# Optimization experiments

Hardware: AMD Instinct MI355X
Metric: run time of the kernel (lower is better)

Reference implementation:

```python
import jax, jax.numpy as jnp
import numpy as np

ALPHA = 0.2  # LeakyReLU negative slope
NEG_BIG = -9e15


def setup_inputs() -> dict:
    key = jax.random.key(0)
    k1, k2, k3, k4 = jax.random.split(key, 4)
    bs, N, Fin, Fout = 4, 4096, 256, 256
    inp = jax.random.normal(k1, (bs, N, Fin), dtype=jnp.float32)
    adj = jax.random.randint(k2, (bs, N, N), 0, 2, dtype=jnp.int32)
    W = jax.random.normal(k3, (Fin, Fout), dtype=jnp.float32) * (1.414 / np.sqrt(Fin))
    a = jax.random.normal(k4, (2 * Fout, 1), dtype=jnp.float32) * 0.1
    return {"input": inp, "adj": adj, "W": W, "a": a}


def reference(input, adj, W, a):
    # h: [bs, N, Fout]
    h = jnp.matmul(input, W)
    Fout = W.shape[1]
    a1 = a[:Fout, 0]   # attends to source node i (row of a_input's first half)
    a2 = a[Fout:, 0]   # attends to node j
    # e[b,i,j] = leakyrelu(a1.h_i + a2.h_j); exact decomposition of
    # cat(h_i, h_j) @ a without materializing the [bs, N, N, 2F] tensor.
    f1 = jnp.einsum('bnf,f->bn', h, a1)  # [bs, N]
    f2 = jnp.einsum('bnf,f->bn', h, a2)  # [bs, N]
    e = jax.nn.leaky_relu(f1[:, :, None] + f2[:, None, :], negative_slope=ALPHA)
    logits = jnp.where(adj > 0, e, NEG_BIG)
    # NOTE: original softmaxes over dim=1 (axis of i), faithfully kept.
    attention = jax.nn.softmax(logits, axis=1)
    # dropout p=0.0 (eval mode) -> identity
    h_prime = jnp.matmul(attention, h)  # contract over axis 2
    return jax.nn.elu(h_prime)  # concat=True
```

## Files before the change

kernel.cpp:

```cpp
#include <hip/hip_runtime.h>
#include <cstdint>
#include <cstddef>


#define GAT_ALPHA 0.2f
#define LOG2E 1.4426950408889634f

#if __has_builtin(__builtin_amdgcn_exp2f)
__device__ __forceinline__ float exp2_fast(float x){ return __builtin_amdgcn_exp2f(x); }
#else
__device__ __forceinline__ float exp2_fast(float x){ return exp2f(x); }
#endif

typedef __bf16 bf16x8 __attribute__((ext_vector_type(8)));
typedef __bf16 bf16x4 __attribute__((ext_vector_type(4)));
typedef float  f32x4  __attribute__((ext_vector_type(4)));

__global__ __launch_bounds__(256) void k1_h_gemm(
    const float* __restrict__ inp, const float* __restrict__ W,
    const float* __restrict__ avec, float* __restrict__ h,
    float* __restrict__ f1p, float* __restrict__ f2p)
{
  const int b  = blockIdx.y;
  const int i0 = blockIdx.x * 64;
  const int tid = threadIdx.x;
  const int tr = tid >> 5;
  const int tc = tid & 31;
  __shared__ float Wt[64][256];
  __shared__ float in_t[64][64];
  float acc[8][8];
  #pragma unroll
  for (int r = 0; r < 8; ++r)
    #pragma unroll
    for (int c = 0; c < 8; ++c) acc[r][c] = 0.f;

  const float* inb = inp + (size_t)b * 4096 * 256;
  for (int kt = 0; kt < 4; ++kt) {
    #pragma unroll
    for (int e = 0; e < 16; ++e) {
      int flat4 = e * 256 + tid;
      int kk = flat4 >> 6;
      int ff = (flat4 & 63) * 4;
      *(float4*)&Wt[kk][ff] = *(const float4*)(W + (size_t)(kt*64 + kk) * 256 + ff);
    }
    #pragma unroll
    for (int e = 0; e < 4; ++e) {
      int flat4 = e * 256 + tid;
      int row = flat4 >> 4;
      int col = (flat4 & 15) * 4;
      *(float4*)&in_t[row][col] = *(const float4*)(inb + (size_t)(i0 + row) * 256 + kt*64 + col);
    }
    __syncthreads();
    for (int k = 0; k < 64; ++k) {
      float av[8], bv[8];
      #pragma unroll
      for (int r = 0; r < 8; ++r) av[r] = in_t[tr*8 + r][k];
      float4 b0 = *(float4*)&Wt[k][tc*8];
      float4 b1 = *(float4*)&Wt[k][tc*8 + 4];
      bv[0]=b0.x; bv[1]=b0.y; bv[2]=b0.z; bv[3]=b0.w;
      bv[4]=b1.x; bv[5]=b1.y; bv[6]=b1.z; bv[7]=b1.w;
      #pragma unroll
      for (int r = 0; r < 8; ++r)
        #pragma unroll
        for (int c = 0; c < 8; ++c)
          acc[r][c] = fmaf(av[r], bv[c], acc[r][c]);
    }
    __syncthreads();
  }

  float* hb = h + (size_t)b * 4096 * 256;
  #pragma unroll
  for (int r = 0; r < 8; ++r) {
    int i = i0 + tr*8 + r;
    float4 o0 = make_float4(acc[r][0], acc[r][1], acc[r][2], acc[r][3]);
    float4 o1 = make_float4(acc[r][4], acc[r][5], acc[r][6], acc[r][7]);
    *(float4*)(hb + (size_t)i * 256 + tc*8)     = o0;
    *(float4*)(hb + (size_t)i * 256 + tc*8 + 4) = o1;
  }

  float a1r[8], a2r[8];
  {
    float4 x0 = *(const float4*)(avec + tc*8);
    float4 x1 = *(const float4*)(avec + tc*8 + 4);
    a1r[0]=x0.x; a1r[1]=x0.y; a1r[2]=x0.z; a1r[3]=x0.w;
    a1r[4]=x1.x; a1r[5]=x1.y; a1r[6]=x1.z; a1r[7]=x1.w;
    float4 y0 = *(const float4*)(avec + 256 + tc*8);
    float4 y1 = *(const float4*)(avec + 256 + tc*8 + 4);
    a2r[0]=y0.x; a2r[1]=y0.y; a2r[2]=y0.z; a2r[3]=y0.w;
    a2r[4]=y1.x; a2r[5]=y1.y; a2r[6]=y1.z; a2r[7]=y1.w;
  }
  #pragma unroll
  for (int r = 0; r < 8; ++r) {
    float v1 = 0.f, v2 = 0.f;
    #pragma unroll
    for (int c = 0; c < 8; ++c) { v1 = fmaf(acc[r][c], a1r[c], v1); v2 = fmaf(acc[r][c], a2r[c], v2); }
    #pragma unroll
    for (int off = 16; off >= 1; off >>= 1) {
      v1 += __shfl_xor(v1, off);
      v2 += __shfl_xor(v2, off);
    }
    if (tc == 0) {
      int i = i0 + tr*8 + r;
      f1p[b*4096 + i] = v1 * LOG2E;
      f2p[b*4096 + i] = v2 * LOG2E;
    }
  }
}

__global__ __launch_bounds__(256) void k2_stream(
    const int* __restrict__ adj, const float* __restrict__ f1p, const float* __restrict__ f2p,
    float* __restrict__ Sp, unsigned long long* __restrict__ mask)
{
  const int jt = blockIdx.x, sp = blockIdx.y, b = blockIdx.z;
  const int tid = threadIdx.x;
  const int wv = tid >> 6, lane = tid & 63;
  const int j0 = jt * 1024;
  const int i0 = sp * 64;

  __shared__ float f1s[64];
  if (tid < 64) f1s[tid] = f1p[b*4096 + i0 + tid];
  float f2v[4], s[4];
  #pragma unroll
  for (int g = 0; g < 4; ++g) {
    f2v[g] = f2p[b*4096 + j0 + g*256 + tid];
    s[g] = 0.f;
  }
  __syncthreads();

  const int* adjb = adj + ((size_t)b * 4096 + i0) * 4096 + j0;
  #pragma unroll 4
  for (int ii = 0; ii < 64; ++ii) {
    const float f1v = f1s[ii];
    const int* arow = adjb + (size_t)ii * 4096;
    #pragma unroll
    for (int g = 0; g < 4; ++g) {
      int av = arow[g*256 + tid];
      bool pr = av > 0;
      unsigned long long bal = __ballot(pr);
      if (lane == 0)
        mask[(size_t)(b*4096 + i0 + ii) * 64 + ((j0 + g*256 + wv*64) >> 6)] = bal;
      float t = f1v + f2v[g];
      float e = fmaxf(t, GAT_ALPHA * t);
      float p = exp2_fast(e);
      s[g] += pr ? p : 0.f;
    }
  }
  #pragma unroll
  for (int g = 0; g < 4; ++g)
    Sp[(size_t)sp * 16384 + b*4096 + j0 + g*256 + tid] = s[g];
}

__global__ __launch_bounds__(256) void k3_combine(
    const float* __restrict__ Sp, float* __restrict__ Sfin)
{
  const int c = blockIdx.x * 256 + threadIdx.x;
  float s = 0.f;
  #pragma unroll
  for (int sp = 0; sp < 64; ++sp) s += Sp[(size_t)sp * 16384 + c];
  Sfin[c] = s;
}

__global__ __launch_bounds__(256) void k4_scale_T(
    const float* __restrict__ h, const float* __restrict__ Sfin, __bf16* __restrict__ hst)
{
  const int b = blockIdx.z, f0 = blockIdx.y * 64, j0 = blockIdx.x * 64;
  const int tid = threadIdx.x;
  __shared__ float tile[64][65];
  __shared__ float sinv[64];
  if (tid < 64) {
    float S = Sfin[b*4096 + j0 + tid];
    sinv[tid] = S > 0.f ? 1.f / S : 0.f;
  }
  const float* hb = h + (size_t)b * 4096 * 256;
  #pragma unroll
  for (int e = 0; e < 4; ++e) {
    int flat4 = e * 256 + tid;
    int jj = flat4 >> 4;
    int ff = (flat4 & 15) * 4;
    float4 v = *(const float4*)(hb + (size_t)(j0 + jj) * 256 + f0 + ff);
    tile[jj][ff] = v.x; tile[jj][ff+1] = v.y; tile[jj][ff+2] = v.z; tile[jj][ff+3] = v.w;
  }
  __syncthreads();
  __bf16* hstb = hst + (size_t)b * 256 * 4096;
  #pragma unroll
  for (int e = 0; e < 4; ++e) {
    int flat4 = e * 256 + tid;
    int fr = flat4 >> 4;
    int jj = (flat4 & 15) * 4;
    bf16x4 o;
    #pragma unroll
    for (int q = 0; q < 4; ++q) o[q] = (__bf16)(tile[jj + q][fr] * sinv[jj + q]);
    *(bf16x4*)(hstb + (size_t)(f0 + fr) * 4096 + j0 + jj) = o;
  }
}

__global__ __launch_bounds__(256) void k5_attn_gemm(
    const __bf16* __restrict__ hst, const float* __restrict__ f1p, const float* __restrict__ f2p,
    const unsigned long long* __restrict__ mask, float* __restrict__ out)
{
  const int ft = blockIdx.x, it = blockIdx.y, b = blockIdx.z;
  const int tid = threadIdx.x;
  const int wid = tid >> 6, lane = tid & 63;
  const int wr = wid >> 1, wc = wid & 1;
  const int l15 = lane & 15, h4 = lane >> 4;
  const int i_w = it * 64 + wr * 32;
  const int f_blk = ft * 128;

  __shared__ __align__(16) char smemB[16384];
  __shared__ float f2all[4096];

  #pragma unroll
  for (int e = 0; e < 16; ++e) {
    int idx = e * 256 + tid;
    f2all[idx] = f2p[b*4096 + idx];
  }
  float f1r[2];
  #pragma unroll
  for (int mf = 0; mf < 2; ++mf) f1r[mf] = f1p[b*4096 + i_w + mf*16 + l15];

  f32x4 acc[2][4];
  #pragma unroll
  for (int mf = 0; mf < 2; ++mf)
    #pragma unroll
    for (int nf = 0; nf < 4; ++nf)
      #pragma unroll
      for (int r = 0; r < 4; ++r) acc[mf][nf][r] = 0.f;

  const char* hstB = (const char*)(hst + (size_t)b * 256 * 4096);
  __syncthreads();

  for (int ch = 0; ch < 64; ++ch) {
    const int jc = ch * 64;
    #pragma unroll
    for (int e = 0; e < 4; ++e) {
      int c16 = e * 256 + tid;
      int f = c16 >> 3;
      int w = (c16 & 7) << 4;
      int wsz = w ^ ((f & 7) << 4);
      uint4 v = *(const uint4*)(hstB + ((size_t)(f_blk + f) * 4096 + jc) * 2 + wsz);
      *(uint4*)(smemB + f * 128 + w) = v;
    }
    unsigned long long mw[2];
    #pragma unroll
    for (int mf = 0; mf < 2; ++mf)
      mw[mf] = mask[(size_t)(b*4096 + i_w + mf*16 + l15) * 64 + (jc >> 6)];
    __syncthreads();

    #pragma unroll
    for (int ks = 0; ks < 2; ++ks) {
      bf16x8 bfr[4];
      #pragma unroll
      for (int nf = 0; nf < 4; ++nf) {
        int f_local = wc * 64 + nf * 16 + l15;
        int byteoff = f_local * 128 + ((ks * 64 + h4 * 16) ^ ((f_local & 7) << 4));
        bfr[nf] = *(const bf16x8*)(smemB + byteoff);
      }
      const int jb = jc + ks * 32 + h4 * 8;
      float4 F0 = *(const float4*)&f2all[jb];
      float4 F1 = *(const float4*)&f2all[jb + 4];
      float f2vv[8] = {F0.x,F0.y,F0.z,F0.w,F1.x,F1.y,F1.z,F1.w};
      #pragma unroll
      for (int mf = 0; mf < 2; ++mf) {
        unsigned int bits = (unsigned int)(mw[mf] >> (ks * 32 + h4 * 8)) & 0xFFu;
        float f1v = f1r[mf];
        bf16x8 af;
        #pragma unroll
        for (int r = 0; r < 8; ++r) {
          float t = f1v + f2vv[r];
          float e = fmaxf(t, GAT_ALPHA * t);
          float p = exp2_fast(e);
          af[r] = ((bits >> r) & 1u) ? (__bf16)p : (__bf16)0.f;
        }
        #pragma unroll
        for (int nf = 0; nf < 4; ++nf)
          acc[mf][nf] = __builtin_amdgcn_mfma_f32_16x16x32_bf16(af, bfr[nf], acc[mf][nf], 0, 0, 0);
      }
    }
    __syncthreads();
  }

  float* outb = out + (size_t)b * 4096 * 256;
  #pragma unroll
  for (int mf = 0; mf < 2; ++mf)
    #pragma unroll
    for (int nf = 0; nf < 4; ++nf)
      #pragma unroll
      for (int r = 0; r < 4; ++r) {
        float x = acc[mf][nf][r];
        float o = x > 0.f ? x : __expf(x) - 1.f;
        int i = i_w + mf * 16 + h4 * 4 + r;
        int f = f_blk + wc * 64 + nf * 16 + l15;
        outb[(size_t)i * 256 + f] = o;
      }
}

extern "C" void kernel_launch(void* const* d_in, const int* in_sizes, int n_in,
                              void* d_out, int out_size, void* d_ws, size_t ws_size,
                              hipStream_t stream) {
  const float* inp  = (const float*)d_in[0];
  const int*   adj  = (const int*)d_in[1];
  const float* W    = (const float*)d_in[2];
  const float* avec = (const float*)d_in[3];
  float* out = (float*)d_out;
  char* ws = (char*)d_ws;

  float* h    = (float*)(ws);
  __bf16* hst = (__bf16*)(ws + 16777216);
  unsigned long long* mask = (unsigned long long*)(ws + 25165824);
  float* f1p  = (float*)(ws + 33554432);
  float* f2p  = (float*)(ws + 33619968);
  float* Sfin = (float*)(ws + 33685504);
  float* Sp   = (float*)(ws + 33751040);

  k1_h_gemm<<<dim3(64, 4), 256, 0, stream>>>(inp, W, avec, h, f1p, f2p);
  k2_stream<<<dim3(4, 64, 4), 256, 0, stream>>>(adj, f1p, f2p, Sp, mask);
  k3_combine<<<64, 256, 0, stream>>>(Sp, Sfin);
  k4_scale_T<<<dim3(64, 4, 4), 256, 0, stream>>>(h, Sfin, hst);
  k5_attn_gemm<<<dim3(2, 64, 4), 256, 0, stream>>>(hst, f1p, f2p, mask, out);
}
```

Before: 644.8 us.

## Move projection GEMM to bf16 MFMA and vectorize adjacency streaming

```diff
diff --git a/kernel.cpp b/kernel.cpp
--- a/kernel.cpp
+++ b/kernel.cpp
@@ -15,139 +15,186 @@
 typedef __bf16 bf16x8 __attribute__((ext_vector_type(8)));
 typedef __bf16 bf16x4 __attribute__((ext_vector_type(4)));
 typedef float  f32x4  __attribute__((ext_vector_type(4)));
-
-__global__ __launch_bounds__(256) void k1_h_gemm(
-    const float* __restrict__ inp, const float* __restrict__ W,
-    const float* __restrict__ avec, float* __restrict__ h,
+typedef unsigned long long ull;
+
+__global__ __launch_bounds__(256) void k0_prep(
+    const float* __restrict__ W, __bf16* __restrict__ Wt)
+{
+  const int f0 = blockIdx.x * 64, k0 = blockIdx.y * 64;
+  const int tid = threadIdx.x;
+  __shared__ float tile[64][65];
+  #pragma unroll
+  for (int e = 0; e < 4; ++e) {
+    int flat4 = e * 256 + tid;
+    int kk = flat4 >> 4;
+    int ff = (flat4 & 15) * 4;
+    float4 v = *(const float4*)(W + (size_t)(k0 + kk) * 256 + f0 + ff);
+    tile[kk][ff] = v.x; tile[kk][ff+1] = v.y; tile[kk][ff+2] = v.z; tile[kk][ff+3] = v.w;
+  }
+  __syncthreads();
+  #pragma unroll
+  for (int e = 0; e < 4; ++e) {
+    int flat4 = e * 256 + tid;
+    int fr = flat4 >> 4;
+    int kk = (flat4 & 15) * 4;
+    bf16x4 o;
+    #pragma unroll
+    for (int q = 0; q < 4; ++q) o[q] = (__bf16)tile[kk + q][fr];
+    *(bf16x4*)(Wt + (size_t)(f0 + fr) * 256 + k0 + kk) = o;
+  }
+}
+
+__global__ __launch_bounds__(256) void k1_mfma(
+    const float* __restrict__ inp, const __bf16* __restrict__ Wt,
+    __bf16* __restrict__ hbf)
+{
+  const int b = blockIdx.y, i0 = blockIdx.x * 64;
+  const int tid = threadIdx.x;
+  const int wid = tid >> 6, lane = tid & 63;
+  const int wr = wid >> 1, wc = wid & 1;
+  const int l15 = lane & 15, h4 = lane >> 4;
+
+  __shared__ __align__(16) char Xs[8192];
+  __shared__ __align__(16) char Ws[32768];
+
+  f32x4 acc[2][8];
+  #pragma unroll
+  for (int mf = 0; mf < 2; ++mf)
+    #pragma unroll
+    for (int nf = 0; nf < 8; ++nf)
+      #pragma unroll
+      for (int q = 0; q < 4; ++q) acc[mf][nf][q] = 0.f;
+
+  const float* inb = inp + (size_t)b * 4096 * 256;
+  const char* WtB = (const char*)Wt;
+
+  for (int kt = 0; kt < 4; ++kt) {
+    {
+      int rX = tid >> 2;
+      int ks16 = (tid & 3) * 16;
+      const float* src = inb + (size_t)(i0 + rX) * 256 + kt * 64 + ks16;
+      float4 v0 = *(const float4*)(src);
+      float4 v1 = *(const float4*)(src + 4);
+      float4 v2 = *(const float4*)(src + 8);
+      float4 v3 = *(const float4*)(src + 12);
+      bf16x8 lo, hi;
+      lo[0]=(__bf16)v0.x; lo[1]=(__bf16)v0.y; lo[2]=(__bf16)v0.z; lo[3]=(__bf16)v0.w;
+      lo[4]=(__bf16)v1.x; lo[5]=(__bf16)v1.y; lo[6]=(__bf16)v1.z; lo[7]=(__bf16)v1.w;
+      hi[0]=(__bf16)v2.x; hi[1]=(__bf16)v2.y; hi[2]=(__bf16)v2.z; hi[3]=(__bf16)v2.w;
+      hi[4]=(__bf16)v3.x; hi[5]=(__bf16)v3.y; hi[6]=(__bf16)v3.z; hi[7]=(__bf16)v3.w;
+      int swz = (rX & 7) << 4;
+      *(bf16x8*)(Xs + rX * 128 + ((ks16 * 2) ^ swz))      = lo;
+      *(bf16x8*)(Xs + rX * 128 + ((ks16 * 2 + 16) ^ swz)) = hi;
+    }
+    #pragma unroll
+    for (int e = 0; e < 8; ++e) {
+      int c16 = e * 256 + tid;
+      int f = c16 >> 3;
+      int sg = c16 & 7;
+      uint4 v = *(const uint4*)(WtB + (size_t)f * 512 + kt * 128 + sg * 16);
+      *(uint4*)(Ws + f * 128 + ((sg * 16) ^ ((f & 7) << 4))) = v;
+    }
+    __syncthreads();
+    #pragma unroll
+    for (int ks = 0; ks < 2; ++ks) {
+      bf16x8 afr[2];
+      #pragma unroll
+      for (int mf = 0; mf < 2; ++mf) {
+        int row = wr * 32 + mf * 16 + l15;
+        afr[mf] = *(const bf16x8*)(Xs + row * 128 + ((ks * 64 + h4 * 16) ^ ((row & 7) << 4)));
+      }
+      bf16x8 bfr[8];
+      #pragma unroll
+      for (int nf = 0; nf < 8; ++nf) {
+        int f = wc * 128 + nf * 16 + l15;
+        bfr[nf] = *(const bf16x8*)(Ws + f * 128 + ((ks * 64 + h4 * 16) ^ ((f & 7) << 4)));
+      }
+      #pragma unroll
+      for (int mf = 0; mf < 2; ++mf)
+        #pragma unroll
+        for (int nf = 0; nf < 8; ++nf)
+          acc[mf][nf] = __builtin_amdgcn_mfma_f32_16x16x32_bf16(afr[mf], bfr[nf], acc[mf][nf], 0, 0, 0);
+    }
+    __syncthreads();
+  }
+
+  __bf16* hb = hbf + ((size_t)b * 4096 + i0) * 256;
+  #pragma unroll
+  for (int mf = 0; mf < 2; ++mf)
+    #pragma unroll
+    for (int nf = 0; nf < 8; ++nf)
+      #pragma unroll
+      for (int q = 0; q < 4; ++q) {
+        int i_loc = wr * 32 + mf * 16 + h4 * 4 + q;
+        int f = wc * 128 + nf * 16 + l15;
+        hb[(size_t)i_loc * 256 + f] = (__bf16)acc[mf][nf][q];
+      }
+}
+
+__global__ __launch_bounds__(256) void k15_f12(
+    const __bf16* __restrict__ hbf, const float* __restrict__ avec,
     float* __restrict__ f1p, float* __restrict__ f2p)
 {
-  const int b  = blockIdx.y;
-  const int i0 = blockIdx.x * 64;
-  const int tid = threadIdx.x;
-  const int tr = tid >> 5;
-  const int tc = tid & 31;
-  __shared__ float Wt[64][256];
-  __shared__ float in_t[64][64];
-  float acc[8][8];
-  #pragma unroll
-  for (int r = 0; r < 8; ++r)
-    #pragma unroll
-    for (int c = 0; c < 8; ++c) acc[r][c] = 0.f;
-
-  const float* inb = inp + (size_t)b * 4096 * 256;
-  for (int kt = 0; kt < 4; ++kt) {
-    #pragma unroll
-    for (int e = 0; e < 16; ++e) {
-      int flat4 = e * 256 + tid;
-      int kk = flat4 >> 6;
-      int ff = (flat4 & 63) * 4;
-      *(float4*)&Wt[kk][ff] = *(const float4*)(W + (size_t)(kt*64 + kk) * 256 + ff);
-    }
-    #pragma unroll
-    for (int e = 0; e < 4; ++e) {
-      int flat4 = e * 256 + tid;
-      int row = flat4 >> 4;
-      int col = (flat4 & 15) * 4;
-      *(float4*)&in_t[row][col] = *(const float4*)(inb + (size_t)(i0 + row) * 256 + kt*64 + col);
-    }
-    __syncthreads();
-    for (int k = 0; k < 64; ++k) {
-      float av[8], bv[8];
-      #pragma unroll
-      for (int r = 0; r < 8; ++r) av[r] = in_t[tr*8 + r][k];
-      float4 b0 = *(float4*)&Wt[k][tc*8];
-      float4 b1 = *(float4*)&Wt[k][tc*8 + 4];
-      bv[0]=b0.x; bv[1]=b0.y; bv[2]=b0.z; bv[3]=b0.w;
-      bv[4]=b1.x; bv[5]=b1.y; bv[6]=b1.z; bv[7]=b1.w;
-      #pragma unroll
-      for (int r = 0; r < 8; ++r)
-        #pragma unroll
-        for (int c = 0; c < 8; ++c)
-          acc[r][c] = fmaf(av[r], bv[c], acc[r][c]);
-    }
-    __syncthreads();
-  }
-
-  float* hb = h + (size_t)b * 4096 * 256;
-  #pragma unroll
-  for (int r = 0; r < 8; ++r) {
-    int i = i0 + tr*8 + r;
-    float4 o0 = make_float4(acc[r][0], acc[r][1], acc[r][2], acc[r][3]);
-    float4 o1 = make_float4(acc[r][4], acc[r][5], acc[r][6], acc[r][7]);
-    *(float4*)(hb + (size_t)i * 256 + tc*8)     = o0;
-    *(float4*)(hb + (size_t)i * 256 + tc*8 + 4) = o1;
-  }
-
-  float a1r[8], a2r[8];
-  {
-    float4 x0 = *(const float4*)(avec + tc*8);
-    float4 x1 = *(const float4*)(avec + tc*8 + 4);
-    a1r[0]=x0.x; a1r[1]=x0.y; a1r[2]=x0.z; a1r[3]=x0.w;
-    a1r[4]=x1.x; a1r[5]=x1.y; a1r[6]=x1.z; a1r[7]=x1.w;
-    float4 y0 = *(const float4*)(avec + 256 + tc*8);
-    float4 y1 = *(const float4*)(avec + 256 + tc*8 + 4);
-    a2r[0]=y0.x; a2r[1]=y0.y; a2r[2]=y0.z; a2r[3]=y0.w;
-    a2r[4]=y1.x; a2r[5]=y1.y; a2r[6]=y1.z; a2r[7]=y1.w;
-  }
-  #pragma unroll
-  for (int r = 0; r < 8; ++r) {
-    float v1 = 0.f, v2 = 0.f;
-    #pragma unroll
-    for (int c = 0; c < 8; ++c) { v1 = fmaf(acc[r][c], a1r[c], v1); v2 = fmaf(acc[r][c], a2r[c], v2); }
-    #pragma unroll
-    for (int off = 16; off >= 1; off >>= 1) {
-      v1 += __shfl_xor(v1, off);
-      v2 += __shfl_xor(v2, off);
-    }
-    if (tc == 0) {
-      int i = i0 + tr*8 + r;
-      f1p[b*4096 + i] = v1 * LOG2E;
-      f2p[b*4096 + i] = v2 * LOG2E;
-    }
-  }
-}
-
-__global__ __launch_bounds__(256) void k2_stream(
+  const int tid = threadIdx.x;
+  const int row = blockIdx.x * 4 + (tid >> 6);
+  const int lane = tid & 63;
+  bf16x4 hv = *(const bf16x4*)(hbf + (size_t)row * 256 + lane * 4);
+  float4 a1 = *(const float4*)(avec + lane * 4);
+  float4 a2 = *(const float4*)(avec + 256 + lane * 4);
+  float v1 = (float)hv[0]*a1.x + (float)hv[1]*a1.y + (float)hv[2]*a1.z + (float)hv[3]*a1.w;
+  float v2 = (float)hv[0]*a2.x + (float)hv[1]*a2.y + (float)hv[2]*a2.z + (float)hv[3]*a2.w;
+  #pragma unroll
+  for (int off = 32; off >= 1; off >>= 1) {
+    v1 += __shfl_xor(v1, off);
+    v2 += __shfl_xor(v2, off);
+  }
+  if (lane == 0) {
+    f1p[row] = v1 * LOG2E;
+    f2p[row] = v2 * LOG2E;
+  }
+}
+
+__global__ __launch_bounds__(128) void k2_stream(
     const int* __restrict__ adj, const float* __restrict__ f1p, const float* __restrict__ f2p,
-    float* __restrict__ Sp, unsigned long long* __restrict__ mask)
-{
-  const int jt = blockIdx.x, sp = blockIdx.y, b = blockIdx.z;
+    float* __restrict__ Sp, ull* __restrict__ maskw)
+{
+  const int jt8 = blockIdx.x, sp = blockIdx.y, b = blockIdx.z;
   const int tid = threadIdx.x;
   const int wv = tid >> 6, lane = tid & 63;
-  const int j0 = jt * 1024;
+  const int grp = jt8 * 2 + wv;
   const int i0 = sp * 64;
 
   __shared__ float f1s[64];
-  if (tid < 64) f1s[tid] = f1p[b*4096 + i0 + tid];
-  float f2v[4], s[4];
-  #pragma unroll
-  for (int g = 0; g < 4; ++g) {
-    f2v[g] = f2p[b*4096 + j0 + g*256 + tid];
-    s[g] = 0.f;
-  }
+  if (tid < 64) f1s[tid] = f1p[b * 4096 + i0 + tid];
+
+  float4 f2v = *(const float4*)(f2p + b * 4096 + grp * 256 + lane * 4);
+  float s0 = 0.f, s1 = 0.f, s2 = 0.f, s3 = 0.f;
   __syncthreads();
 
-  const int* adjb = adj + ((size_t)b * 4096 + i0) * 4096 + j0;
-  #pragma unroll 4
+  const int* adjb = adj + ((size_t)b * 4096 + i0) * 4096 + grp * 256 + lane * 4;
+  #pragma unroll 8
   for (int ii = 0; ii < 64; ++ii) {
+    int4 av = *(const int4*)(adjb + (size_t)ii * 4096);
     const float f1v = f1s[ii];
-    const int* arow = adjb + (size_t)ii * 4096;
-    #pragma unroll
-    for (int g = 0; g < 4; ++g) {
-      int av = arow[g*256 + tid];
-      bool pr = av > 0;
-      unsigned long long bal = __ballot(pr);
-      if (lane == 0)
-        mask[(size_t)(b*4096 + i0 + ii) * 64 + ((j0 + g*256 + wv*64) >> 6)] = bal;
-      float t = f1v + f2v[g];
-      float e = fmaxf(t, GAT_ALPHA * t);
-      float p = exp2_fast(e);
-      s[g] += pr ? p : 0.f;
-    }
-  }
-  #pragma unroll
-  for (int g = 0; g < 4; ++g)
-    Sp[(size_t)sp * 16384 + b*4096 + j0 + g*256 + tid] = s[g];
+    bool p0 = av.x > 0, p1 = av.y > 0, p2 = av.z > 0, p3 = av.w > 0;
+    ull b0 = __ballot(p0), b1 = __ballot(p1), b2 = __ballot(p2), b3 = __ballot(p3);
+    if (lane == 0) {
+      size_t wbase = ((size_t)(b * 4096 + i0 + ii) * 16 + grp) * 4;
+      ulonglong2 m01; m01.x = b0; m01.y = b1;
+      ulonglong2 m23; m23.x = b2; m23.y = b3;
+      *(ulonglong2*)(maskw + wbase)     = m01;
+      *(ulonglong2*)(maskw + wbase + 2) = m23;
+    }
+    float t0 = f1v + f2v.x, t1 = f1v + f2v.y, t2 = f1v + f2v.z, t3 = f1v + f2v.w;
+    float e0 = fmaxf(t0, GAT_ALPHA * t0), e1 = fmaxf(t1, GAT_ALPHA * t1);
+    float e2 = fmaxf(t2, GAT_ALPHA * t2), e3 = fmaxf(t3, GAT_ALPHA * t3);
+    s0 += p0 ? exp2_fast(e0) : 0.f;
+    s1 += p1 ? exp2_fast(e1) : 0.f;
+    s2 += p2 ? exp2_fast(e2) : 0.f;
+    s3 += p3 ? exp2_fast(e3) : 0.f;
+  }
+  float4 sv; sv.x = s0; sv.y = s1; sv.z = s2; sv.w = s3;
+  *(float4*)(Sp + (size_t)sp * 16384 + b * 4096 + grp * 256 + lane * 4) = sv;
 }
 
 __global__ __launch_bounds__(256) void k3_combine(
@@ -161,24 +208,25 @@
 }
 
 __global__ __launch_bounds__(256) void k4_scale_T(
-    const float* __restrict__ h, const float* __restrict__ Sfin, __bf16* __restrict__ hst)
+    const __bf16* __restrict__ hbf, const float* __restrict__ Sfin, __bf16* __restrict__ hst)
 {
   const int b = blockIdx.z, f0 = blockIdx.y * 64, j0 = blockIdx.x * 64;
   const int tid = threadIdx.x;
   __shared__ float tile[64][65];
   __shared__ float sinv[64];
   if (tid < 64) {
-    float S = Sfin[b*4096 + j0 + tid];
+    float S = Sfin[b * 4096 + j0 + tid];
     sinv[tid] = S > 0.f ? 1.f / S : 0.f;
   }
-  const float* hb = h + (size_t)b * 4096 * 256;
-  #pragma unroll
-  for (int e = 0; e < 4; ++e) {
-    int flat4 = e * 256 + tid;
-    int jj = flat4 >> 4;
-    int ff = (flat4 & 15) * 4;
-    float4 v = *(const float4*)(hb + (size_t)(j0 + jj) * 256 + f0 + ff);
-    tile[jj][ff] = v.x; tile[jj][ff+1] = v.y; tile[jj][ff+2] = v.z; tile[jj][ff+3] = v.w;
+  const __bf16* hb = hbf + (size_t)b * 4096 * 256;
+  #pragma unroll
+  for (int e = 0; e < 2; ++e) {
+    int flat8 = e * 256 + tid;
+    int jj = flat8 >> 3;
+    int ff = (flat8 & 7) * 8;
+    bf16x8 v = *(const bf16x8*)(hb + (size_t)(j0 + jj) * 256 + f0 + ff);
+    #pragma unroll
+    for (int q = 0; q < 8; ++q) tile[jj][ff + q] = (float)v[q];
   }
   __syncthreads();
   __bf16* hstb = hst + (size_t)b * 256 * 4096;
@@ -196,7 +244,7 @@
 
 __global__ __launch_bounds__(256) void k5_attn_gemm(
     const __bf16* __restrict__ hst, const float* __restrict__ f1p, const float* __restrict__ f2p,
-    const unsigned long long* __restrict__ mask, float* __restrict__ out)
+    const ull* __restrict__ maskw, float* __restrict__ out)
 {
   const int ft = blockIdx.x, it = blockIdx.y, b = blockIdx.z;
   const int tid = threadIdx.x;
@@ -212,11 +260,11 @@
   #pragma unroll
   for (int e = 0; e < 16; ++e) {
     int idx = e * 256 + tid;
-    f2all[idx] = f2p[b*4096 + idx];
+    f2all[idx] = f2p[b * 4096 + idx];
   }
   float f1r[2];
   #pragma unroll
-  for (int mf = 0; mf < 2; ++mf) f1r[mf] = f1p[b*4096 + i_w + mf*16 + l15];
+  for (int mf = 0; mf < 2; ++mf) f1r[mf] = f1p[b * 4096 + i_w + mf * 16 + l15];
 
   f32x4 acc[2][4];
   #pragma unroll
@@ -224,59 +272,67 @@
     #pragma unroll
     for (int nf = 0; nf < 4; ++nf)
       #pragma unroll
-      for (int r = 0; r < 4; ++r) acc[mf][nf][r] = 0.f;
+      for (int q = 0; q < 4; ++q) acc[mf][nf][q] = 0.f;
 
   const char* hstB = (const char*)(hst + (size_t)b * 256 * 4096);
   __syncthreads();
 
-  for (int ch = 0; ch < 64; ++ch) {
-    const int jc = ch * 64;
-    #pragma unroll
-    for (int e = 0; e < 4; ++e) {
-      int c16 = e * 256 + tid;
-      int f = c16 >> 3;
-      int w = (c16 & 7) << 4;
-      int wsz = w ^ ((f & 7) << 4);
-      uint4 v = *(const uint4*)(hstB + ((size_t)(f_blk + f) * 4096 + jc) * 2 + wsz);
-      *(uint4*)(smemB + f * 128 + w) = v;
-    }
-    unsigned long long mw[2];
-    #pragma unroll
-    for (int mf = 0; mf < 2; ++mf)
-      mw[mf] = mask[(size_t)(b*4096 + i_w + mf*16 + l15) * 64 + (jc >> 6)];
-    __syncthreads();
-
-    #pragma unroll
-    for (int ks = 0; ks < 2; ++ks) {
-      bf16x8 bfr[4];
-      #pragma unroll
-      for (int nf = 0; nf < 4; ++nf) {
-        int f_local = wc * 64 + nf * 16 + l15;
-        int byteoff = f_local * 128 + ((ks * 64 + h4 * 16) ^ ((f_local & 7) << 4));
-        bfr[nf] = *(const bf16x8*)(smemB + byteoff);
-      }
-      const int jb = jc + ks * 32 + h4 * 8;
-      float4 F0 = *(const float4*)&f2all[jb];
-      float4 F1 = *(const float4*)&f2all[jb + 4];
-      float f2vv[8] = {F0.x,F0.y,F0.z,F0.w,F1.x,F1.y,F1.z,F1.w};
-      #pragma unroll
-      for (int mf = 0; mf < 2; ++mf) {
-        unsigned int bits = (unsigned int)(mw[mf] >> (ks * 32 + h4 * 8)) & 0xFFu;
-        float f1v = f1r[mf];
-        bf16x8 af;
+  for (int g16 = 0; g16 < 16; ++g16) {
+    ull w0[2], w1[2], w2[2], w3[2];
+    #pragma unroll
+    for (int mf = 0; mf < 2; ++mf) {
+      size_t base = ((size_t)(b * 4096 + i_w + mf * 16 + l15) * 16 + g16) * 4;
+      ulonglong2 p01 = *(const ulonglong2*)(maskw + base);
+      ulonglong2 p23 = *(const ulonglong2*)(maskw + base + 2);
+      w0[mf] = p01.x; w1[mf] = p01.y; w2[mf] = p23.x; w3[mf] = p23.y;
+    }
+    #pragma unroll 1
+    for (int cb = 0; cb < 4; ++cb) {
+      const int jc = g16 * 256 + cb * 64;
+      #pragma unroll
+      for (int e = 0; e < 4; ++e) {
+        int c16 = e * 256 + tid;
+        int f = c16 >> 3;
+        int w = (c16 & 7) << 4;
+        int wsz = w ^ ((f & 7) << 4);
+        uint4 v = *(const uint4*)(hstB + ((size_t)(f_blk + f) * 4096 + jc) * 2 + wsz);
+        *(uint4*)(smemB + f * 128 + w) = v;
+      }
+      __syncthreads();
+
+      #pragma unroll
+      for (int ks = 0; ks < 2; ++ks) {
+        bf16x8 bfr[4];
         #pragma unroll
-        for (int r = 0; r < 8; ++r) {
-          float t = f1v + f2vv[r];
-          float e = fmaxf(t, GAT_ALPHA * t);
-          float p = exp2_fast(e);
-          af[r] = ((bits >> r) & 1u) ? (__bf16)p : (__bf16)0.f;
+        for (int nf = 0; nf < 4; ++nf) {
+          int f_local = wc * 64 + nf * 16 + l15;
+          int byteoff = f_local * 128 + ((ks * 64 + h4 * 16) ^ ((f_local & 7) << 4));
+          bfr[nf] = *(const bf16x8*)(smemB + byteoff);
         }
+        const int jb = jc + ks * 32 + h4 * 8;
+        float4 F0 = *(const float4*)&f2all[jb];
+        float4 F1 = *(const float4*)&f2all[jb + 4];
+        float f2vv[8] = {F0.x, F0.y, F0.z, F0.w, F1.x, F1.y, F1.z, F1.w};
+        const int sh0 = cb * 16 + ks * 8 + h4 * 2;
         #pragma unroll
-        for (int nf = 0; nf < 4; ++nf)
-          acc[mf][nf] = __builtin_amdgcn_mfma_f32_16x16x32_bf16(af, bfr[nf], acc[mf][nf], 0, 0, 0);
-      }
-    }
-    __syncthreads();
+        for (int mf = 0; mf < 2; ++mf) {
+          float f1v = f1r[mf];
+          bf16x8 af;
+          #pragma unroll
+          for (int r = 0; r < 8; ++r) {
+            float t = f1v + f2vv[r];
+            float e = fmaxf(t, GAT_ALPHA * t);
+            float p = exp2_fast(e);
+            ull wsel = (r & 3) == 0 ? w0[mf] : (r & 3) == 1 ? w1[mf] : (r & 3) == 2 ? w2[mf] : w3[mf];
+            af[r] = ((wsel >> (sh0 + (r >> 2))) & 1ull) ? (__bf16)p : (__bf16)0.f;
+          }
+          #pragma unroll
+          for (int nf = 0; nf < 4; ++nf)
+            acc[mf][nf] = __builtin_amdgcn_mfma_f32_16x16x32_bf16(af, bfr[nf], acc[mf][nf], 0, 0, 0);
+        }
+      }
+      __syncthreads();
+    }
   }
 
   float* outb = out + (size_t)b * 4096 * 256;
@@ -285,10 +341,10 @@
     #pragma unroll
     for (int nf = 0; nf < 4; ++nf)
       #pragma unroll
-      for (int r = 0; r < 4; ++r) {
-        float x = acc[mf][nf][r];
+      for (int q = 0; q < 4; ++q) {
+        float x = acc[mf][nf][q];
         float o = x > 0.f ? x : __expf(x) - 1.f;
-        int i = i_w + mf * 16 + h4 * 4 + r;
+        int i = i_w + mf * 16 + h4 * 4 + q;
         int f = f_blk + wc * 64 + nf * 16 + l15;
         outb[(size_t)i * 256 + f] = o;
       }
@@ -304,17 +360,20 @@
   float* out = (float*)d_out;
   char* ws = (char*)d_ws;
 
-  float* h    = (float*)(ws);
-  __bf16* hst = (__bf16*)(ws + 16777216);
-  unsigned long long* mask = (unsigned long long*)(ws + 25165824);
-  float* f1p  = (float*)(ws + 33554432);
-  float* f2p  = (float*)(ws + 33619968);
-  float* Sfin = (float*)(ws + 33685504);
-  float* Sp   = (float*)(ws + 33751040);
-
-  k1_h_gemm<<<dim3(64, 4), 256, 0, stream>>>(inp, W, avec, h, f1p, f2p);
-  k2_stream<<<dim3(4, 64, 4), 256, 0, stream>>>(adj, f1p, f2p, Sp, mask);
+  __bf16* hbf  = (__bf16*)(ws);
+  __bf16* hst  = (__bf16*)(ws + 8388608);
+  ull*    maskw= (ull*)   (ws + 16777216);
+  __bf16* Wt   = (__bf16*)(ws + 25165824);
+  float*  f1p  = (float*) (ws + 25296896);
+  float*  f2p  = (float*) (ws + 25362432);
+  float*  Sfin = (float*) (ws + 25427968);
+  float*  Sp   = (float*) (ws + 25493504);
+
+  k0_prep<<<dim3(4, 4), 256, 0, stream>>>(W, Wt);
+  k1_mfma<<<dim3(64, 4), 256, 0, stream>>>(inp, Wt, hbf);
+  k15_f12<<<4096, 256, 0, stream>>>(hbf, avec, f1p, f2p);
+  k2_stream<<<dim3(8, 64, 4), 128, 0, stream>>>(adj, f1p, f2p, Sp, maskw);
   k3_combine<<<64, 256, 0, stream>>>(Sp, Sfin);
-  k4_scale_T<<<dim3(64, 4, 4), 256, 0, stream>>>(h, Sfin, hst);
-  k5_attn_gemm<<<dim3(2, 64, 4), 256, 0, stream>>>(hst, f1p, f2p, mask, out);
-}
+  k4_scale_T<<<dim3(64, 4, 4), 256, 0, stream>>>(hbf, Sfin, hst);
+  k5_attn_gemm<<<dim3(2, 64, 4), 256, 0, stream>>>(hst, f1p, f2p, maskw, out);
+}
```

After: 562.4 us. -12.8%, faster.
